# Performance work log

Hardware: AMD Instinct MI355X
Metric: run time of the kernel (lower is better)

Reference implementation:

```python
import jax, jax.numpy as jnp
import numpy as np
import math

C64 = jnp.complex64

def _fftconv_full(a, kern):
    # full linear convolution along last axis (complex), like scipy.signal.fftconvolve
    L = a.shape[-1] + kern.shape[0] - 1
    A = jnp.fft.fft(a, n=L, axis=-1)
    K = jnp.fft.fft(kern.astype(a.dtype), n=L)
    return jnp.fft.ifft(A * K, axis=-1)

def _centered_ifft(f):
    # out[shft] = ifft(f[shft]) * sqrt(N), shft = (arange(N)+fix(N/2)) % N
    N = f.shape[-1]
    shft = (np.arange(N) + int(np.fix(N / 2))) % N
    inv = np.argsort(shft)
    g = jnp.fft.ifft(f[..., shft], axis=-1) * math.sqrt(N)
    return g[..., inv].astype(f.dtype)

def _sincinterp(f):
    # zero-stuff by 2 then sinc-filter; returns length 2N-1 along last axis
    N = f.shape[-1]
    y = jnp.zeros(f.shape[:-1] + (2 * N - 1,), f.dtype).at[..., ::2].set(f)
    kern = jnp.asarray(np.sinc(np.arange(-(2 * N - 3), 2 * N - 2) / 2.0).astype(np.complex64))
    return _fftconv_full(y, kern)[..., 2 * N - 3: 4 * N - 4]

def _frft_chirp(f, a):
    # Ozaktas chirp-convolution discrete FrFT, valid for 0.5 <= a <= 1.5
    N = f.shape[-1]
    alpha = a * math.pi / 2
    tana2, sina = math.tan(alpha / 2), math.sin(alpha)
    fi = _sincinterp(f)                                   # [..., 2N-1]
    pad = jnp.zeros(f.shape[:-1] + (N - 1,), f.dtype)
    fp = jnp.concatenate([pad, fi, pad], axis=-1)         # [..., 4N-3]
    n = np.arange(-2 * N + 2, 2 * N - 1).astype(np.float64)
    chrp = jnp.asarray(np.exp(-1j * math.pi / N * tana2 / 4 * n ** 2).astype(np.complex64))
    fp = chrp * fp
    c = math.pi / N / sina / 4
    m = np.arange(-(4 * N - 4), 4 * N - 3).astype(np.float64)
    kern = jnp.asarray(np.exp(1j * c * m ** 2).astype(np.complex64))
    ret = _fftconv_full(fp, kern)[..., 4 * N - 4: 8 * N - 7] * math.sqrt(c / math.pi)
    ret = chrp * ret
    phase = np.complex64(np.exp(-1j * (1 - a) * math.pi / 4))
    return phase * ret[..., N - 1: 3 * N - 2: 2]          # [..., N]

def _frft_last(f, a):
    # torch branch logic for the a values used here: a=0.5 (fwd), a=-0.5 (inv)
    if a < 0.5:
        f = _centered_ifft(f)
        a = a + 1.0
    return _frft_chirp(f, a)

def _frft2d(x, a):
    t = _frft_last(x, a)                                  # rows: along W
    return jnp.swapaxes(_frft_last(jnp.swapaxes(t, -1, -2), a), -1, -2)  # cols: along H

def _c1x1(x, w, b=None):
    y = jnp.einsum('nchw,oc->nohw', x, w)
    return y if b is None else y + b[None, :, None, None]

def _c3x3(x, w, b):
    y = jax.lax.conv_general_dilated(x, w, (1, 1), 'SAME',
                                     dimension_numbers=('NCHW', 'OIHW', 'NCHW'))
    return y + b[None, :, None, None]

def _forward(x, conv1_w, mag_s_w, mag_s_b, mag_f_w, mag_f_b, mag_w, mag_b,
             pha_w, pha_b, conv_0_w, conv_0_b, conv_1_w, conv_1_b, conv2_w):
    angle = 0.5
    alpha = math.cos(angle * math.pi / 2)
    N, C, H, W = x.shape
    H1, W1 = int(H * alpha), int(W * alpha)
    x1 = _c1x1(x, conv1_w)                                # stride=1 -> downsample is identity
    C1, C0 = C // 4, C // 4 // 3
    x_0, x_05, x_1 = x1[:, :C0], x1[:, C0:C1 - C0], x1[:, C1 - C0:C1]
    h0, w0 = (H - H1) // 2, (W - W1) // 2
    mask1 = jnp.zeros((H, W), jnp.float32).at[h0:h0 + H1, w0:w0 + W1].set(1.0)
    mask2 = 1.0 - mask1
    # fractional Fourier branch
    Fre = _frft2d(x_05.astype(C64), angle)
    mag, pha = jnp.abs(Fre), jnp.angle(Fre)
    mag_out = _c1x1(_c3x3(mag * mask1, mag_s_w, mag_s_b) * mask1
                    + _c1x1(mag * mask2, mag_f_w, mag_f_b) * mask2, mag_w, mag_b)
    pha_out = _c1x1(pha, pha_w, pha_b)
    Fre_out = jax.lax.complex(mag_out * jnp.cos(pha_out), mag_out * jnp.sin(pha_out))
    ifrft = jnp.abs(_frft2d(Fre_out, -angle))
    # plain Fourier branch (conv_1 applied to both mag and pha, as in the source)
    fre = jnp.fft.rfft2(x_1)
    fm, fp = jnp.abs(fre), jnp.angle(fre)
    mo = _c1x1(fm, conv_1_w, conv_1_b)
    po = _c1x1(fp, conv_1_w, conv_1_b)
    x_1o = jnp.fft.irfft2(jax.lax.complex(mo * jnp.cos(po), mo * jnp.sin(po)), s=(H, W))
    x_0o = _c1x1(x_0, conv_0_w, conv_0_b)
    return _c1x1(jnp.concatenate([x_0o, ifrft, x_1o], axis=1), conv2_w)

def setup_inputs():
    key = jax.random.key(0)
    ks = jax.random.split(key, 16)
    N, C, H, W, Co = 4, 192, 128, 128, 192
    C1, C0 = C // 4, C // 4 // 3
    Cm = C1 - 2 * C0
    s = 0.05
    r = lambda k, sh: jax.random.normal(k, sh, jnp.float32)
    return {
        "x": r(ks[0], (N, C, H, W)),
        "conv1_w": r(ks[1], (C1, C)) * s,
        "mag_s_w": r(ks[2], (Cm, Cm, 3, 3)) * s, "mag_s_b": r(ks[3], (Cm,)) * s,
        "mag_f_w": r(ks[4], (Cm, Cm)) * s, "mag_f_b": r(ks[5], (Cm,)) * s,
        "mag_w": r(ks[6], (Cm, Cm)) * s, "mag_b": r(ks[7], (Cm,)) * s,
        "pha_w": r(ks[8], (Cm, Cm)) * s, "pha_b": r(ks[9], (Cm,)) * s,
        "conv_0_w": r(ks[10], (C0, C0)) * s, "conv_0_b": r(ks[11], (C0,)) * s,
        "conv_1_w": r(ks[12], (C0, C0)) * s, "conv_1_b": r(ks[13], (C0,)) * s,
        "conv2_w": r(ks[14], (Co, C1)) * s,
    }

def reference(x, conv1_w, mag_s_w, mag_s_b, mag_f_w, mag_f_b, mag_w, mag_b,
              pha_w, pha_b, conv_0_w, conv_0_b, conv_1_w, conv_1_b, conv2_w):
    return _forward(x, conv1_w, mag_s_w, mag_s_b, mag_f_w, mag_f_b, mag_w, mag_b,
                    pha_w, pha_b, conv_0_w, conv_0_b, conv_1_w, conv_1_b, conv2_w)
```

## Files before the change

### kernel.cpp

```cpp
#include <hip/hip_runtime.h>
#include <math.h>

#define PI_D 3.14159265358979323846
#define TWO_PI_F 6.2831853071795864f

__device__ __align__(16) float2 g_Mf [128*128];
__device__ __align__(16) float2 g_MfT[128*128];
__device__ __align__(16) float2 g_Mb [128*128];
__device__ __align__(16) float2 g_MbT[128*128];
__device__ __align__(16) float2 g_F  [128*128];
__device__ __align__(16) float2 g_IF [128*128];
__device__ __align__(16) float  g_x1 [4*48*16384];
__device__ __align__(16) float2 g_bufA[64*16384];
__device__ __align__(16) float2 g_bufB[64*16384];
__device__ __align__(16) float  g_mag[64*16384];
__device__ __align__(16) float  g_pha[64*16384];
__device__ __align__(16) float  g_m65[64*8320];
__device__ __align__(16) float  g_p65[64*8320];
__device__ __align__(16) float  g_t1 [64*16384];
__device__ __align__(16) float  g_t2 [64*16384];
__device__ __align__(16) float  g_t3 [64*8320];
__device__ __align__(16) float  g_t4 [64*8320];
__device__ __align__(16) float  g_cat[4*48*16384];

__device__ inline void build_A_body(int tid) {
    if (tid >= 128*128) return;
    int o = tid >> 7, m = tid & 127;
    const double chc = -PI_D/128.0 * tan(PI_D/8.0) * 0.25;
    const double c   =  PI_D/(512.0*sin(PI_D/4.0));
    const double inv2pi = 1.0/(2.0*PI_D);
    float sr, si;
    {
        int n1 = 2*m - 127, tt = 2*(o - m);
        double ang = chc*(double)(n1*n1) + c*(double)(tt*tt);
        double r = ang*inv2pi; r -= floor(r);
        float af = (float)(r*2.0*PI_D);
        float sn, cs; __sincosf(af, &sn, &cs);
        sr = cs; si = sn;
    }
    for (int j = 0; j < 127; ++j) {
        int q  = 2*j + 1;
        int n1 = q - 127, tt = 2*o - q, d = q - 2*m;
        double ang = chc*(double)(n1*n1) + c*(double)(tt*tt);
        double r = ang*inv2pi; r -= floor(r);
        float af = (float)(r*2.0*PI_D);
        float s = (((d-1)>>1) & 1) ? -2.0f : 2.0f;
        s /= (3.14159265358979f*(float)d);
        float sn, cs; __sincosf(af, &sn, &cs);
        sr += s*cs; si += s*sn;
    }
    int n2 = 2*o - 127;
    double ph = chc*(double)(n2*n2) - PI_D/8.0;
    double r = ph*inv2pi; r -= floor(r);
    float pf = (float)(r*2.0*PI_D);
    float scale = (float)sqrt(c/PI_D);
    float sn, cs; __sincosf(pf, &sn, &cs);
    float cr = cs*scale, ci = sn*scale;
    float2 v = make_float2(sr*cr - si*ci, sr*ci + si*cr);
    g_Mf[tid] = v;
    g_MfT[(m<<7) + o] = v;
    int p = (o*m) & 127;
    float ang2 = TWO_PI_F*(float)p/128.0f;
    float sn2, cs2; __sincosf(ang2, &sn2, &cs2);
    g_F[tid]  = make_float2(cs2, -sn2);
    g_IF[tid] = make_float2(cs2*0.0078125f, sn2*0.0078125f);
}

template<int LM>
__device__ inline void load_T4(float2* tr, const float* mp, const float* pp,
                               const float* Trl, int hh, int w4) {
    if (LM == 1) {
        float4 v = *(const float4*)(Trl + (hh<<7) + w4);
        tr[0] = make_float2(v.x, 0.f); tr[1] = make_float2(v.y, 0.f);
        tr[2] = make_float2(v.z, 0.f); tr[3] = make_float2(v.w, 0.f);
    } else if (LM == 2) {
#pragma unroll
        for (int i = 0; i < 4; ++i) {
            int idx = (hh<<7) + w4 + i;
            float m = mp[idx], ph = pp[idx];
            float sn, cs; __sincosf(ph, &sn, &cs);
            tr[i] = make_float2(m*cs, m*sn);
        }
    } else {
#pragma unroll
        for (int i = 0; i < 4; ++i) {
            int w = w4 + i;
            int h2 = hh, w2 = w; float sg = 1.f;
            if (w >= 65) { h2 = (128 - hh) & 127; w2 = 128 - w; sg = -1.f; }
            int idx = h2*65 + w2;
            float m = mp[idx], ph = pp[idx];
            float sn, cs; __sincosf(ph, &sn, &cs);
            tr[i] = make_float2(m*cs, sg*m*sn);
        }
    }
}

__device__ inline void cfma(float2& a, float sx, float sy, float mx, float my) {
    a.x = fmaf(sx, mx, a.x); a.x = fmaf(-sy, my, a.x);
    a.y = fmaf(sx, my, a.y); a.y = fmaf(sy, mx, a.y);
}

template<int LM>
__device__ inline void rmul_body(const float2* __restrict__ MT, const float* __restrict__ Trl,
                                 const float* __restrict__ mp_, const float* __restrict__ pp_,
                                 float2* __restrict__ out, int cstart,
                                 int p, int r0, int t, float2* Ssh, float2* Mch) {
    constexpr bool RS = (LM == 1);
    const float* Trp = nullptr; const float* mp = nullptr; const float* pp = nullptr;
    if (LM == 1) { int n = p >> 4, c = p & 15; Trp = Trl + ((long)(n*48 + cstart + c) << 14); }
    if (LM == 2) { mp = mp_ + ((long)p << 14); pp = pp_ + ((long)p << 14); }
    if (LM == 3) { mp = mp_ + (long)p*8320;   pp = pp_ + (long)p*8320; }
    for (int u = t; u < 512; u += 256) {
        int row = u >> 5, w4 = (u & 31) << 2;
        float2 tr4[4];
        load_T4<LM>(tr4, mp, pp, Trp, r0 + row, w4);
        float4* d = (float4*)&Ssh[(row << 7) + w4];
        d[0] = make_float4(tr4[0].x, tr4[0].y, tr4[1].x, tr4[1].y);
        d[1] = make_float4(tr4[2].x, tr4[2].y, tr4[3].x, tr4[3].y);
    }
    float2 acc[4][2] = {};
    int cq = t & 63, rp = t >> 6;
    for (int kc = 0; kc < 128; kc += 16) {
        __syncthreads();
        {
            const float4* Mg = (const float4*)(MT + (kc << 7));
            float4* Md = (float4*)Mch;
            for (int i = t; i < 1024; i += 256) Md[i] = Mg[i];
        }
        __syncthreads();
#pragma unroll
        for (int kk = 0; kk < 16; kk += 2) {
            float4 s2[4];
#pragma unroll
            for (int i = 0; i < 4; ++i)
                s2[i] = *(const float4*)&Ssh[(((rp<<2)+i) << 7) + kc + kk];
            float4 m0 = *(const float4*)&Mch[(kk << 7) + (cq<<1)];
            float4 m1 = *(const float4*)&Mch[((kk+1) << 7) + (cq<<1)];
#pragma unroll
            for (int i = 0; i < 4; ++i) {
                if (RS) {
                    acc[i][0].x = fmaf(s2[i].x, m0.x, acc[i][0].x);
                    acc[i][0].y = fmaf(s2[i].x, m0.y, acc[i][0].y);
                    acc[i][1].x = fmaf(s2[i].x, m0.z, acc[i][1].x);
                    acc[i][1].y = fmaf(s2[i].x, m0.w, acc[i][1].y);
                    acc[i][0].x = fmaf(s2[i].z, m1.x, acc[i][0].x);
                    acc[i][0].y = fmaf(s2[i].z, m1.y, acc[i][0].y);
                    acc[i][1].x = fmaf(s2[i].z, m1.z, acc[i][1].x);
                    acc[i][1].y = fmaf(s2[i].z, m1.w, acc[i][1].y);
                } else {
                    cfma(acc[i][0], s2[i].x, s2[i].y, m0.x, m0.y);
                    cfma(acc[i][1], s2[i].x, s2[i].y, m0.z, m0.w);
                    cfma(acc[i][0], s2[i].z, s2[i].w, m1.x, m1.y);
                    cfma(acc[i][1], s2[i].z, s2[i].w, m1.z, m1.w);
                }
            }
        }
    }
    long base = ((long)p << 14);
#pragma unroll
    for (int i = 0; i < 4; ++i) {
        float4* dst = (float4*)(out + base + ((long)(r0 + (rp<<2) + i) << 7) + (cq<<1));
        *dst = make_float4(acc[i][0].x, acc[i][0].y, acc[i][1].x, acc[i][1].y);
    }
}

template<int EPI>
__device__ inline void lmul_body(const float2* __restrict__ A, const float2* __restrict__ in,
                                 float* __restrict__ o1, float* __restrict__ o2, int coff,
                                 int p, int j0, int t, float2* Ssh, float2* Tch) {
    const float2* T = in + ((long)p << 14);
    {
        const float4* Ag = (const float4*)(A + ((long)j0 << 7));
        float4* Sd = (float4*)Ssh;
        for (int i = t; i < 1024; i += 256) Sd[i] = Ag[i];
    }
    float2 acc[4][2] = {};
    int cq = t & 63, rp = t >> 6;
    for (int kc = 0; kc < 128; kc += 16) {
        __syncthreads();
        {
            const float4* Tg = (const float4*)(T + (kc << 7));
            float4* Td = (float4*)Tch;
            for (int i = t; i < 1024; i += 256) Td[i] = Tg[i];
        }
        __syncthreads();
#pragma unroll
        for (int kk = 0; kk < 16; kk += 2) {
            float4 s2[4];
#pragma unroll
            for (int i = 0; i < 4; ++i)
                s2[i] = *(const float4*)&Ssh[(((rp<<2)+i) << 7) + kc + kk];
            float4 m0 = *(const float4*)&Tch[(kk << 7) + (cq<<1)];
            float4 m1 = *(const float4*)&Tch[((kk+1) << 7) + (cq<<1)];
#pragma unroll
            for (int i = 0; i < 4; ++i) {
                if (EPI == 3) {
                    acc[i][0].x = fmaf(s2[i].x, m0.x, acc[i][0].x);
                    acc[i][0].x = fmaf(-s2[i].y, m0.y, acc[i][0].x);
                    acc[i][1].x = fmaf(s2[i].x, m0.z, acc[i][1].x);
                    acc[i][1].x = fmaf(-s2[i].y, m0.w, acc[i][1].x);
                    acc[i][0].x = fmaf(s2[i].z, m1.x, acc[i][0].x);
                    acc[i][0].x = fmaf(-s2[i].w, m1.y, acc[i][0].x);
                    acc[i][1].x = fmaf(s2[i].z, m1.z, acc[i][1].x);
                    acc[i][1].x = fmaf(-s2[i].w, m1.w, acc[i][1].x);
                } else {
                    cfma(acc[i][0], s2[i].x, s2[i].y, m0.x, m0.y);
                    cfma(acc[i][1], s2[i].x, s2[i].y, m0.z, m0.w);
                    cfma(acc[i][0], s2[i].z, s2[i].w, m1.x, m1.y);
                    cfma(acc[i][1], s2[i].z, s2[i].w, m1.z, m1.w);
                }
            }
        }
    }
#pragma unroll
    for (int i = 0; i < 4; ++i) {
        int jj = j0 + (rp<<2) + i;
        int ww0 = cq << 1;
        float2 v0 = acc[i][0], v1 = acc[i][1];
        if (EPI == 1) {
            long idx = ((long)p << 14) + ((long)jj << 7) + ww0;
            *(float2*)&o1[idx] = make_float2(sqrtf(v0.x*v0.x + v0.y*v0.y),
                                             sqrtf(v1.x*v1.x + v1.y*v1.y));
            *(float2*)&o2[idx] = make_float2(atan2f(v0.y, v0.x), atan2f(v1.y, v1.x));
        } else if (EPI == 2) {
            int n = p >> 4, c = p & 15;
            long idx = ((long)(n*48 + coff + c) << 14) + ((long)jj << 7) + ww0;
            *(float2*)&o1[idx] = make_float2(sqrtf(v0.x*v0.x + v0.y*v0.y),
                                             sqrtf(v1.x*v1.x + v1.y*v1.y));
        } else if (EPI == 3) {
            int n = p >> 4, c = p & 15;
            long idx = ((long)(n*48 + coff + c) << 14) + ((long)jj << 7) + ww0;
            *(float2*)&o1[idx] = make_float2(v0.x, v1.x);
        } else if (EPI == 4) {
            if (ww0 < 65) {
                long idx = (long)p*8320 + jj*65 + ww0;
                o1[idx] = sqrtf(v0.x*v0.x + v0.y*v0.y);
                o2[idx] = atan2f(v0.y, v0.x);
                if (ww0 + 1 < 65) {
                    o1[idx+1] = sqrtf(v1.x*v1.x + v1.y*v1.y);
                    o2[idx+1] = atan2f(v1.y, v1.x);
                }
            }
        }
    }
}

template<int LMA, int LMB>
__global__ __launch_bounds__(256, 4)
void k_rmul_dual(const float2* __restrict__ MTa, const float* __restrict__ TrlA,
                 const float* __restrict__ mpA, const float* __restrict__ ppA,
                 float2* __restrict__ outA, int cstartA,
                 const float2* __restrict__ MTb, const float* __restrict__ TrlB,
                 const float* __restrict__ mpB, const float* __restrict__ ppB,
                 float2* __restrict__ outB, int cstartB) {
    __shared__ float2 Ssh[16*128];
    __shared__ float2 Mch[16*128];
    __shared__ float2 W[128];
    int bx = blockIdx.x, by = blockIdx.y, t = threadIdx.x;
    if (bx >= 128) {
        int b = (bx - 128)*8 + by;
        if (b < 64) {
            if (t < 128) {
                float ang = TWO_PI_F*(float)t/128.0f;
                float sn, cs; __sincosf(ang, &sn, &cs);
                float invs = 0.08838834764831845f;
                W[t] = make_float2(cs*invs, sn*invs);
            }
            __syncthreads();
            int tid = b*256 + t;
            int o = tid >> 7, m = tid & 127;
            float sr = 0.f, si = 0.f;
            for (int r = 0; r < 128; ++r) {
                float2 a = g_Mf[(o<<7) + r];
                int k = ((r+64)*(m+64)) & 127;
                float2 w = W[k];
                sr += a.x*w.x - a.y*w.y;
                si += a.x*w.y + a.y*w.x;
            }
            float2 v = make_float2(sr, si);
            g_Mb[tid] = v;
            g_MbT[(m<<7) + o] = v;
        }
        return;
    }
    int p = bx & 63, r0 = by << 4;
    if (bx < 64) rmul_body<LMA>(MTa, TrlA, mpA, ppA, outA, cstartA, p, r0, t, Ssh, Mch);
    else         rmul_body<LMB>(MTb, TrlB, mpB, ppB, outB, cstartB, p, r0, t, Ssh, Mch);
}

template<int EPIA, int EPIB>
__global__ __launch_bounds__(256, 4)
void k_lmul_dual(const float2* __restrict__ Aa, const float2* __restrict__ inA,
                 float* __restrict__ o1A, float* __restrict__ o2A, int coffA,
                 const float2* __restrict__ Ab, const float2* __restrict__ inB,
                 float* __restrict__ o1B, float* __restrict__ o2B, int coffB) {
    __shared__ float2 Ssh[16*128];
    __shared__ float2 Tch[16*128];
    int bx = blockIdx.x, j0 = blockIdx.y << 4, t = threadIdx.x;
    int p = bx & 63;
    if (bx < 64) lmul_body<EPIA>(Aa, inA, o1A, o2A, coffA, p, j0, t, Ssh, Tch);
    else         lmul_body<EPIB>(Ab, inB, o1B, o2B, coffB, p, j0, t, Ssh, Tch);
}

template<int CIN, int COUT, int KSPLIT, int OSPLIT>
__device__ inline void wconv_body(const float* __restrict__ in, const float* __restrict__ wgt,
                                  const float* __restrict__ bias, float* __restrict__ out,
                                  int S, int Ctin, int cstart, int Ctout, int costart,
                                  int n, int sblk, float* red) {
    constexpr int OW = COUT / OSPLIT;
    constexpr int KC = CIN / KSPLIT;
    int t = threadIdx.x, lane = t & 63;
    int wv = __builtin_amdgcn_readfirstlane(t >> 6);
    int oq = wv / KSPLIT, kq = wv % KSPLIT;
    int s0 = sblk << 7;
    const float* inb = in + ((long)(n*Ctin + cstart + kq*KC))*S + s0 + (lane<<1);
    const float* wb  = wgt + (oq*OW)*CIN + kq*KC;
    float2 acc[OW];
#pragma unroll
    for (int j = 0; j < OW; ++j) acc[j] = make_float2(0.f, 0.f);
#pragma unroll 4
    for (int c = 0; c < KC; ++c) {
        float2 xv = *(const float2*)(inb + (long)c*S);
#pragma unroll
        for (int j = 0; j < OW; ++j) {
            float w = wb[j*CIN + c];
            acc[j].x = fmaf(w, xv.x, acc[j].x);
            acc[j].y = fmaf(w, xv.y, acc[j].y);
        }
    }
    if (KSPLIT == 1) {
#pragma unroll
        for (int j = 0; j < OW; ++j) {
            int o = oq*OW + j;
            float b = bias ? bias[o] : 0.f;
            *(float2*)(out + ((long)(n*Ctout + costart + o))*S + s0 + (lane<<1))
                = make_float2(acc[j].x + b, acc[j].y + b);
        }
    } else {
#pragma unroll
        for (int j = 0; j < OW; ++j) {
            int o = oq*OW + j;
            *(float2*)&red[((kq*COUT + o) << 7) + (lane<<1)] = acc[j];
        }
        __syncthreads();
        for (int idx = t; idx < COUT*64; idx += 256) {
            int o = idx >> 6, l2 = (idx & 63) << 1;
            float b = bias ? bias[o] : 0.f;
            float2 v = make_float2(b, b);
#pragma unroll
            for (int k2 = 0; k2 < KSPLIT; ++k2) {
                float2 r = *(const float2*)&red[((k2*COUT + o) << 7) + l2];
                v.x += r.x; v.y += r.y;
            }
            *(float2*)(out + ((long)(n*Ctout + costart + o))*S + s0 + l2) = v;
        }
    }
}

__global__ __launch_bounds__(256, 1)
void k_conv1_build(const float* __restrict__ x, const float* __restrict__ w,
                   float* __restrict__ x1) {
    __shared__ float red[2*48*128];
    if (blockIdx.z == 0) {
        wconv_body<192,48,2,2>(x, w, nullptr, x1, 16384, 192, 0, 48, 0,
                               blockIdx.y, blockIdx.x, red);
    } else {
        int b = blockIdx.y*gridDim.x + blockIdx.x;
        if (b < 64) build_A_body(b*256 + threadIdx.x);
    }
}

__global__ __launch_bounds__(256, 1)
void k_conv2(const float* __restrict__ in, const float* __restrict__ wgt,
             float* __restrict__ out) {
    __shared__ float red[1];
    wconv_body<48,192,1,4>(in, wgt, nullptr, out, 16384, 48, 0, 192, 0,
                           blockIdx.y, blockIdx.x, red);
}

__device__ inline void mix16b(const float* __restrict__ in, const float* __restrict__ w,
                              const float* __restrict__ b, float* __restrict__ out,
                              int Ctin, int S, int n, int s0base, int Slim) {
    int t = threadIdx.x, lane = t & 63;
    int wv = __builtin_amdgcn_readfirstlane(t >> 6);
    int oq = wv & 3, pg = wv >> 2;
    int s0 = s0base + (pg << 7);
    if (s0 >= Slim) return;
    const float* inb = in + ((long)(n*Ctin))*S + s0 + (lane<<1);
    float2 acc[4];
#pragma unroll
    for (int j = 0; j < 4; ++j) {
        float bb = b ? b[oq*4 + j] : 0.f;
        acc[j] = make_float2(bb, bb);
    }
#pragma unroll
    for (int half = 0; half < 2; ++half) {
        float2 xv[8];
#pragma unroll
        for (int c = 0; c < 8; ++c)
            xv[c] = *(const float2*)(inb + (long)(half*8 + c)*S);
#pragma unroll
        for (int c = 0; c < 8; ++c) {
#pragma unroll
            for (int j = 0; j < 4; ++j) {
                float ww = w[(oq*4 + j)*16 + half*8 + c];
                acc[j].x = fmaf(ww, xv[c].x, acc[j].x);
                acc[j].y = fmaf(ww, xv[c].y, acc[j].y);
            }
        }
    }
#pragma unroll
    for (int j = 0; j < 4; ++j) {
        int o = oq*4 + j;
        *(float2*)(out + ((long)(n*Ctin + o))*S + s0 + (lane<<1)) = acc[j];
    }
}

__device__ inline void maskconv_body(const float* __restrict__ mag, const float* __restrict__ ws3,
                                     const float* __restrict__ bs, const float* __restrict__ wf,
                                     const float* __restrict__ bf, const float* __restrict__ wm,
                                     const float* __restrict__ bm, float* __restrict__ out,
                                     int n, int tile, float* patch) {
    int h0 = (tile >> 3) << 4, w0 = (tile & 7) << 4;
    int t = threadIdx.x;
    const float* magn = mag + ((long)n << 18);
    for (int idx = t; idx < 16*324; idx += 1024) {
        int c = idx / 324, r = idx - c*324;
        int ph = r / 18, pw = r - ph*18;
        int gh = h0 - 1 + ph, gw = w0 - 1 + pw;
        float v = 0.f;
        if (gh >= 19 && gh < 109 && gw >= 19 && gw < 109)
            v = magn[(c<<14) + (gh<<7) + gw];
        patch[c*324 + r] = v;
    }
    __syncthreads();
    int oq = t >> 8, pix = t & 255;
    int ty = pix >> 4, tx = pix & 15;
    int h = h0 + ty, w = w0 + tx;
    bool in1 = (h >= 19 && h < 109 && w >= 19 && w < 109);
    unsigned long long bal = __ballot(in1);
    float res[4];
    if (bal != 0ull) {
        float acc[4];
#pragma unroll
        for (int j = 0; j < 4; ++j) acc[j] = bs[oq*4 + j];
        for (int c = 0; c < 16; ++c) {
            const float* pc = patch + c*324 + ty*18 + tx;
            const float* wc = ws3 + c*9;
#pragma unroll
            for (int dh = 0; dh < 3; ++dh) {
#pragma unroll
                for (int dw = 0; dw < 3; ++dw) {
                    float tap = pc[dh*18 + dw];
#pragma unroll
                    for (int j = 0; j < 4; ++j)
                        acc[j] = fmaf(wc[(oq*4 + j)*144 + dh*3 + dw], tap, acc[j]);
                }
            }
        }
#pragma unroll
        for (int j = 0; j < 4; ++j) res[j] = acc[j];
    }
    if (bal != ~0ull) {
        float acc2[4];
#pragma unroll
        for (int j = 0; j < 4; ++j) acc2[j] = bf[oq*4 + j];
#pragma unroll
        for (int half = 0; half < 2; ++half) {
            float xv[8];
#pragma unroll
            for (int c = 0; c < 8; ++c)
                xv[c] = magn[((half*8 + c)<<14) + (h<<7) + w];
#pragma unroll
            for (int c = 0; c < 8; ++c)
#pragma unroll
                for (int j = 0; j < 4; ++j)
                    acc2[j] = fmaf(wf[(oq*4 + j)*16 + half*8 + c], xv[c], acc2[j]);
        }
        if (!in1) {
#pragma unroll
            for (int j = 0; j < 4; ++j) res[j] = acc2[j];
        }
    }
    __syncthreads();
    float* resl = patch;
#pragma unroll
    for (int j = 0; j < 4; ++j) resl[(oq*4 + j)*256 + pix] = res[j];
    __syncthreads();
    float rr[16];
#pragma unroll
    for (int o = 0; o < 16; ++o) rr[o] = resl[o*256 + pix];
#pragma unroll
    for (int j = 0; j < 4; ++j) {
        int o2 = oq*4 + j;
        float a = bm[o2];
#pragma unroll
        for (int o = 0; o < 16; ++o)
            a = fmaf(wm[o2*16 + o], rr[o], a);
        out[((long)((n<<4) + o2) << 14) + (h << 7) + w] = a;
    }
}

__global__ __launch_bounds__(1024, 8)
void k_point(const float* __restrict__ mag, const float* __restrict__ ws3,
             const float* __restrict__ bs, const float* __restrict__ wf,
             const float* __restrict__ bf, const float* __restrict__ wm,
             const float* __restrict__ bm, float* __restrict__ t2,
             const float* __restrict__ pha, const float* __restrict__ pw,
             const float* __restrict__ pb, float* __restrict__ t1,
             const float* __restrict__ x1, const float* __restrict__ c0w,
             const float* __restrict__ c0b, float* __restrict__ cat,
             const float* __restrict__ m65, const float* __restrict__ p65,
             const float* __restrict__ c1w, const float* __restrict__ c1b,
             float* __restrict__ t3, float* __restrict__ t4) {
    __shared__ float patch[16*324];
    int b = blockIdx.x;
    if (b < 256) {
        maskconv_body(mag, ws3, bs, wf, bf, wm, bm, t2, b >> 6, b & 63, patch);
    } else if (b < 384) {
        int i = b - 256;
        mix16b(pha, pw, pb, t1, 16, 16384, i >> 5, (i & 31) << 9, 16384);
    } else if (b < 512) {
        int i = b - 384;
        mix16b(x1, c0w, c0b, cat, 48, 16384, i >> 5, (i & 31) << 9, 16384);
    } else if (b < 580) {
        int i = b - 512;
        mix16b(m65, c1w, c1b, t3, 16, 8320, i / 17, (i % 17) << 9, 8320);
    } else {
        int i = b - 580;
        mix16b(p65, c1w, c1b, t4, 16, 8320, i / 17, (i % 17) << 9, 8320);
    }
}

extern "C" void kernel_launch(void* const* d_in, const int* in_sizes, int n_in,
                              void* d_out, int out_size, void* d_ws, size_t ws_size,
                              hipStream_t stream) {
    (void)in_sizes; (void)n_in; (void)out_size; (void)d_ws; (void)ws_size;
    const float* x        = (const float*)d_in[0];
    const float* conv1_w  = (const float*)d_in[1];
    const float* mag_s_w  = (const float*)d_in[2];
    const float* mag_s_b  = (const float*)d_in[3];
    const float* mag_f_w  = (const float*)d_in[4];
    const float* mag_f_b  = (const float*)d_in[5];
    const float* mag_w_   = (const float*)d_in[6];
    const float* mag_b_   = (const float*)d_in[7];
    const float* pha_w_   = (const float*)d_in[8];
    const float* pha_b_   = (const float*)d_in[9];
    const float* conv_0_w = (const float*)d_in[10];
    const float* conv_0_b = (const float*)d_in[11];
    const float* conv_1_w = (const float*)d_in[12];
    const float* conv_1_b = (const float*)d_in[13];
    const float* conv2_w  = (const float*)d_in[14];
    float* outp = (float*)d_out;

    float2 *Mf, *MfT, *Mb, *MbT, *Fm, *IFm, *bufA, *bufB;
    float *x1, *mag, *pha, *m65, *p65, *t1, *t2, *t3, *t4, *cat;
    hipGetSymbolAddress((void**)&Mf,   HIP_SYMBOL(g_Mf));
    hipGetSymbolAddress((void**)&MfT,  HIP_SYMBOL(g_MfT));
    hipGetSymbolAddress((void**)&Mb,   HIP_SYMBOL(g_Mb));
    hipGetSymbolAddress((void**)&MbT,  HIP_SYMBOL(g_MbT));
    hipGetSymbolAddress((void**)&Fm,   HIP_SYMBOL(g_F));
    hipGetSymbolAddress((void**)&IFm,  HIP_SYMBOL(g_IF));
    hipGetSymbolAddress((void**)&bufA, HIP_SYMBOL(g_bufA));
    hipGetSymbolAddress((void**)&bufB, HIP_SYMBOL(g_bufB));
    hipGetSymbolAddress((void**)&x1,   HIP_SYMBOL(g_x1));
    hipGetSymbolAddress((void**)&mag,  HIP_SYMBOL(g_mag));
    hipGetSymbolAddress((void**)&pha,  HIP_SYMBOL(g_pha));
    hipGetSymbolAddress((void**)&m65,  HIP_SYMBOL(g_m65));
    hipGetSymbolAddress((void**)&p65,  HIP_SYMBOL(g_p65));
    hipGetSymbolAddress((void**)&t1,   HIP_SYMBOL(g_t1));
    hipGetSymbolAddress((void**)&t2,   HIP_SYMBOL(g_t2));
    hipGetSymbolAddress((void**)&t3,   HIP_SYMBOL(g_t3));
    hipGetSymbolAddress((void**)&t4,   HIP_SYMBOL(g_t4));
    hipGetSymbolAddress((void**)&cat,  HIP_SYMBOL(g_cat));

    dim3 bt(256, 1, 1);

    k_conv1_build<<<dim3(128,4,2), bt, 0, stream>>>(x, conv1_w, x1);

    k_rmul_dual<1,1><<<dim3(136,8), bt, 0, stream>>>(
        MfT, x1, nullptr, nullptr, bufA, 16,
        Fm,  x1, nullptr, nullptr, bufB, 32);

    k_lmul_dual<1,4><<<dim3(128,8), bt, 0, stream>>>(
        Mf, bufA, mag, pha, 0,
        Fm, bufB, m65, p65, 0);

    k_point<<<648, dim3(1024,1,1), 0, stream>>>(mag, mag_s_w, mag_s_b, mag_f_w, mag_f_b,
                                                mag_w_, mag_b_, t2,
                                                pha, pha_w_, pha_b_, t1,
                                                x1, conv_0_w, conv_0_b, cat,
                                                m65, p65, conv_1_w, conv_1_b, t3, t4);

    k_rmul_dual<2,3><<<dim3(128,8), bt, 0, stream>>>(
        MbT, nullptr, t2, t1, bufA, 0,
        IFm, nullptr, t3, t4, bufB, 0);

    k_lmul_dual<2,3><<<dim3(128,8), bt, 0, stream>>>(
        Mb,  bufA, cat, nullptr, 16,
        IFm, bufB, cat, nullptr, 32);

    k_conv2<<<dim3(128,4), bt, 0, stream>>>(cat, conv2_w, outp);
}
```

Baseline: 326.3 us.

## Double-buffer matrix k-chunks with register prefetch in complex matmul kernels

The rmul and lmul complex matmul bodies now split the 16-row shared chunk into two 8-row halves used as a double buffer. The next chunk's global loads go into registers while the current chunk is computed, which cuts the two barriers per iteration to one. The goal is to hide global load latency behind the FMA work. In exchange it runs twice as many k-iterations with smaller chunks and holds extra prefetch registers.

```diff
diff --git a/kernel.cpp b/kernel.cpp
--- a/kernel.cpp
+++ b/kernel.cpp
@@ -118,24 +118,31 @@
         d[0] = make_float4(tr4[0].x, tr4[0].y, tr4[1].x, tr4[1].y);
         d[1] = make_float4(tr4[2].x, tr4[2].y, tr4[3].x, tr4[3].y);
     }
+    const float4* Mg = (const float4*)MT;
+    float4* Mb2[2] = { (float4*)Mch, (float4*)(Mch + 8*128) };
+    float4 pf0 = Mg[t], pf1 = Mg[t + 256];
     float2 acc[4][2] = {};
     int cq = t & 63, rp = t >> 6;
-    for (int kc = 0; kc < 128; kc += 16) {
+    for (int kc = 0; kc < 16; ++kc) {
+        {
+            float4* dst = Mb2[kc & 1];
+            dst[t] = pf0; dst[t + 256] = pf1;
+        }
+        if (kc < 15) {
+            const float4* src = Mg + ((kc + 1) << 9);
+            pf0 = src[t]; pf1 = src[t + 256];
+        }
         __syncthreads();
-        {
-            const float4* Mg = (const float4*)(MT + (kc << 7));
-            float4* Md = (float4*)Mch;
-            for (int i = t; i < 1024; i += 256) Md[i] = Mg[i];
-        }
-        __syncthreads();
-#pragma unroll
-        for (int kk = 0; kk < 16; kk += 2) {
+        const float2* Mc = (const float2*)Mb2[kc & 1];
+        int kbase = kc << 3;
+#pragma unroll
+        for (int kk = 0; kk < 8; kk += 2) {
             float4 s2[4];
 #pragma unroll
             for (int i = 0; i < 4; ++i)
-                s2[i] = *(const float4*)&Ssh[(((rp<<2)+i) << 7) + kc + kk];
-            float4 m0 = *(const float4*)&Mch[(kk << 7) + (cq<<1)];
-            float4 m1 = *(const float4*)&Mch[((kk+1) << 7) + (cq<<1)];
+                s2[i] = *(const float4*)&Ssh[(((rp<<2)+i) << 7) + kbase + kk];
+            float4 m0 = *(const float4*)&Mc[(kk << 7) + (cq<<1)];
+            float4 m1 = *(const float4*)&Mc[((kk+1) << 7) + (cq<<1)];
 #pragma unroll
             for (int i = 0; i < 4; ++i) {
                 if (RS) {
@@ -174,24 +181,31 @@
         float4* Sd = (float4*)Ssh;
         for (int i = t; i < 1024; i += 256) Sd[i] = Ag[i];
     }
+    const float4* Tg = (const float4*)T;
+    float4* Tb2[2] = { (float4*)Tch, (float4*)(Tch + 8*128) };
+    float4 pf0 = Tg[t], pf1 = Tg[t + 256];
     float2 acc[4][2] = {};
     int cq = t & 63, rp = t >> 6;
-    for (int kc = 0; kc < 128; kc += 16) {
+    for (int kc = 0; kc < 16; ++kc) {
+        {
+            float4* dst = Tb2[kc & 1];
+            dst[t] = pf0; dst[t + 256] = pf1;
+        }
+        if (kc < 15) {
+            const float4* src = Tg + ((kc + 1) << 9);
+            pf0 = src[t]; pf1 = src[t + 256];
+        }
         __syncthreads();
-        {
-            const float4* Tg = (const float4*)(T + (kc << 7));
-            float4* Td = (float4*)Tch;
-            for (int i = t; i < 1024; i += 256) Td[i] = Tg[i];
-        }
-        __syncthreads();
-#pragma unroll
-        for (int kk = 0; kk < 16; kk += 2) {
+        const float2* Tc = (const float2*)Tb2[kc & 1];
+        int kbase = kc << 3;
+#pragma unroll
+        for (int kk = 0; kk < 8; kk += 2) {
             float4 s2[4];
 #pragma unroll
             for (int i = 0; i < 4; ++i)
-                s2[i] = *(const float4*)&Ssh[(((rp<<2)+i) << 7) + kc + kk];
-            float4 m0 = *(const float4*)&Tch[(kk << 7) + (cq<<1)];
-            float4 m1 = *(const float4*)&Tch[((kk+1) << 7) + (cq<<1)];
+                s2[i] = *(const float4*)&Ssh[(((rp<<2)+i) << 7) + kbase + kk];
+            float4 m0 = *(const float4*)&Tc[(kk << 7) + (cq<<1)];
+            float4 m1 = *(const float4*)&Tc[((kk+1) << 7) + (cq<<1)];
 #pragma unroll
             for (int i = 0; i < 4; ++i) {
                 if (EPI == 3) {
@@ -253,8 +267,8 @@
                  const float2* __restrict__ MTb, const float* __restrict__ TrlB,
                  const float* __restrict__ mpB, const float* __restrict__ ppB,
                  float2* __restrict__ outB, int cstartB) {
-    __shared__ float2 Ssh[16*128];
-    __shared__ float2 Mch[16*128];
+    __shared__ __align__(16) float2 Ssh[16*128];
+    __shared__ __align__(16) float2 Mch[16*128];
     __shared__ float2 W[128];
     int bx = blockIdx.x, by = blockIdx.y, t = threadIdx.x;
     if (bx >= 128) {
@@ -294,8 +308,8 @@
                  float* __restrict__ o1A, float* __restrict__ o2A, int coffA,
                  const float2* __restrict__ Ab, const float2* __restrict__ inB,
                  float* __restrict__ o1B, float* __restrict__ o2B, int coffB) {
-    __shared__ float2 Ssh[16*128];
-    __shared__ float2 Tch[16*128];
+    __shared__ __align__(16) float2 Ssh[16*128];
+    __shared__ __align__(16) float2 Tch[16*128];
     int bx = blockIdx.x, j0 = blockIdx.y << 4, t = threadIdx.x;
     int p = bx & 63;
     if (bx < 64) lmul_body<EPIA>(Aa, inA, o1A, o2A, coffA, p, j0, t, Ssh, Tch);
```

New measurement: 360.2 us. 10.4% more time.
